# Kernel optimization log

Hardware: AMD Instinct MI355X
Metric: run time of the kernel (lower is better)

## Reference

```python
import jax, jax.numpy as jnp
import numpy as np

B, T, C, H = 2, 2048, 768, 12
HD = C // H  # head dim = 64
EPS = 1e-5


def layer_norm(x, g, b):
    mu = jnp.mean(x, axis=-1, keepdims=True)
    var = jnp.var(x, axis=-1, keepdims=True)
    return (x - mu) * jax.lax.rsqrt(var + EPS) * g + b


def setup_inputs() -> dict:
    key = jax.random.key(0)
    ks = jax.random.split(key, 5)
    s = 0.02
    return {
        "x": jax.random.normal(ks[0], (B, T, C), jnp.float32),
        "ln1_g": jnp.ones((C,), jnp.float32),
        "ln1_b": jnp.zeros((C,), jnp.float32),
        "W_qkv": jax.random.normal(ks[1], (C, 3 * C), jnp.float32) * s,
        "W_attn_proj": jax.random.normal(ks[2], (C, C), jnp.float32) * s,
        "ln2_g": jnp.ones((C,), jnp.float32),
        "ln2_b": jnp.zeros((C,), jnp.float32),
        "W_fc": jax.random.normal(ks[3], (C, 4 * C), jnp.float32) * s,
        "W_mlp_proj": jax.random.normal(ks[4], (4 * C, C), jnp.float32) * s,
    }


def attention(x, W_qkv, W_attn_proj):
    b, t, c = x.shape
    qkv = x @ W_qkv  # [B,T,3C]
    q, k, v = jnp.split(qkv, 3, axis=-1)
    # [B,H,T,HD]
    q = q.reshape(b, t, H, HD).transpose(0, 2, 1, 3)
    k = k.reshape(b, t, H, HD).transpose(0, 2, 1, 3)
    v = v.reshape(b, t, H, HD).transpose(0, 2, 1, 3)
    att = jnp.einsum("bhqd,bhkd->bhqk", q, k) * (1.0 / np.sqrt(HD).astype(np.float32))
    causal = jnp.tril(jnp.ones((t, t), jnp.bool_))
    att = jnp.where(causal, att, jnp.finfo(att.dtype).min)
    att = jax.nn.softmax(att, axis=-1)
    y = jnp.einsum("bhqk,bhkd->bhqd", att, v)
    y = y.transpose(0, 2, 1, 3).reshape(b, t, c)
    return y @ W_attn_proj


def mlp(x, W_fc, W_mlp_proj):
    h = jax.nn.gelu(x @ W_fc, approximate=False)
    return h @ W_mlp_proj


def reference(x, ln1_g, ln1_b, W_qkv, W_attn_proj, ln2_g, ln2_b, W_fc, W_mlp_proj):
    x = x + attention(layer_norm(x, ln1_g, ln1_b), W_qkv, W_attn_proj)
    x = x + mlp(layer_norm(x, ln2_g, ln2_b), W_fc, W_mlp_proj)
    return x
```

## Files before the change

kernel.cpp:

```cpp
#include <hip/hip_runtime.h>
#include <cstdint>
#include <cstddef>

typedef unsigned short u16;
typedef __attribute__((ext_vector_type(4))) float f32x4;
typedef __attribute__((ext_vector_type(8))) short bf16x8;

__device__ __forceinline__ u16 f2bf(float f) {
  unsigned int u = __builtin_bit_cast(unsigned int, f);
  u += 0x7fffu + ((u >> 16) & 1u);
  return (u16)(u >> 16);
}

__device__ __forceinline__ void gl_lds16(const u16* g, u16* lds_base) {
  __builtin_amdgcn_global_load_lds(
      (const __attribute__((address_space(1))) unsigned int*)g,
      (__attribute__((address_space(3))) unsigned int*)lds_base, 16, 0, 0);
}

__global__ __launch_bounds__(256) void transpose_all(const float* __restrict__ s0,
                                                     const float* __restrict__ s1,
                                                     const float* __restrict__ s2,
                                                     const float* __restrict__ s3,
                                                     u16* __restrict__ d0,
                                                     u16* __restrict__ d1,
                                                     u16* __restrict__ d2,
                                                     u16* __restrict__ d3) {
  __shared__ float tile[32][33];
  int idx = blockIdx.x;
  const float* src; u16* dst; int K, N, t;
  if (idx < 1728)      { src = s0; dst = d0; K = 768;  N = 2304; t = idx; }
  else if (idx < 2304) { src = s1; dst = d1; K = 768;  N = 768;  t = idx - 1728; }
  else if (idx < 4608) { src = s2; dst = d2; K = 768;  N = 3072; t = idx - 2304; }
  else                 { src = s3; dst = d3; K = 3072; N = 768;  t = idx - 4608; }
  int nt_n = N >> 5;
  int n0 = (t % nt_n) * 32, k0 = (t / nt_n) * 32;
  int tx = threadIdx.x & 31, ty = threadIdx.x >> 5;
#pragma unroll
  for (int i = 0; i < 4; ++i)
    tile[ty + i * 8][tx] = src[(size_t)(k0 + ty + i * 8) * N + n0 + tx];
  __syncthreads();
#pragma unroll
  for (int i = 0; i < 4; ++i)
    dst[(size_t)(n0 + ty + i * 8) * K + k0 + tx] = f2bf(tile[tx][ty + i * 8]);
}

__global__ __launch_bounds__(256) void transpose_v(const u16* __restrict__ qkvb,
                                                   u16* __restrict__ vt,
                                                   unsigned int* __restrict__ ctr) {
  __shared__ u16 tile[64 * 72];
  if (blockIdx.x == 0 && blockIdx.y == 0 && threadIdx.x == 0) *ctr = 0u;
  int t0 = blockIdx.x * 64;
  int bh = blockIdx.y;
  int b = bh / 12, h = bh % 12;
  int tid = threadIdx.x;
  int c8 = tid & 7, r = tid >> 3;
#pragma unroll
  for (int i = 0; i < 2; ++i) {
    int rr = r + i * 32;
    *(uint4*)&tile[rr * 72 + c8 * 8] =
        *(const uint4*)&qkvb[(size_t)(b * 2048 + t0 + rr) * 2304 + 1536 + h * 64 + c8 * 8];
  }
  __syncthreads();
#pragma unroll
  for (int i = 0; i < 2; ++i) {
    int dr = r + i * 32;
    u16 tmp[8];
#pragma unroll
    for (int j = 0; j < 8; ++j) tmp[j] = tile[(c8 * 8 + j) * 72 + dr];
    *(uint4*)&vt[((size_t)bh * 64 + dr) * 2048 + t0 + c8 * 8] = *(uint4*)tmp;
  }
}

__global__ __launch_bounds__(192) void ln_rows(const float* __restrict__ x,
                                               const float* __restrict__ g,
                                               const float* __restrict__ bb,
                                               u16* __restrict__ out) {
  int row = blockIdx.x;
  int t = threadIdx.x;
  float4 v = *(const float4*)(x + (size_t)row * 768 + t * 4);
  float s = v.x + v.y + v.z + v.w;
  float sq = v.x * v.x + v.y * v.y + v.z * v.z + v.w * v.w;
#pragma unroll
  for (int o = 32; o > 0; o >>= 1) {
    s += __shfl_down(s, o);
    sq += __shfl_down(sq, o);
  }
  __shared__ float ss[3], s2[3];
  int w = t >> 6;
  if ((t & 63) == 0) { ss[w] = s; s2[w] = sq; }
  __syncthreads();
  s = ss[0] + ss[1] + ss[2];
  sq = s2[0] + s2[1] + s2[2];
  float mu = s * (1.f / 768.f);
  float var = sq * (1.f / 768.f) - mu * mu;
  float rs = rsqrtf(var + 1e-5f);
  float4 gv = *(const float4*)(g + t * 4);
  float4 bv = *(const float4*)(bb + t * 4);
  u16 o4[4];
  o4[0] = f2bf((v.x - mu) * rs * gv.x + bv.x);
  o4[1] = f2bf((v.y - mu) * rs * gv.y + bv.y);
  o4[2] = f2bf((v.z - mu) * rs * gv.z + bv.z);
  o4[3] = f2bf((v.w - mu) * rs * gv.w + bv.w);
  *(uint2*)(out + (size_t)row * 768 + t * 4) = *(uint2*)o4;
}

template <int EPI, int TM>
__global__ __launch_bounds__(256, 3) void gemm_bt(const u16* __restrict__ A,
                                                  const u16* __restrict__ BT,
                                                  int M, int N, int K,
                                                  float* __restrict__ outF,
                                                  u16* __restrict__ outB,
                                                  const float* __restrict__ res) {
  constexpr int MT = TM / 64;
  __shared__ __align__(16) u16 Al[2][TM * 64];
  __shared__ __align__(16) u16 Bl[2][64 * 64];
  int tid = threadIdx.x;
  int lane = tid & 63, w = tid >> 6;
  int l16 = lane & 15, quad = lane >> 4;
  int swz = l16 & 7;

  int gx = gridDim.x;
  int nwg = gx * gridDim.y;
  int wg = blockIdx.y * gx + blockIdx.x;
  int chunk = nwg >> 3;
  int swg = (wg & 7) * chunk + (wg >> 3);
  int bx = swg % gx, by = swg / gx;

  size_t rowA0 = (size_t)by * TM;
  size_t rowB0 = (size_t)bx * 64;

  auto stage = [&](int buf, int k0) {
#pragma unroll
    for (int i = 0; i < TM / 32; ++i) {
      int cbase = (i * 4 + w) * 64;
      int chunk2 = cbase + lane;
      int r = chunk2 >> 3, c8 = (chunk2 & 7) ^ (r & 7);
      gl_lds16(&A[(rowA0 + r) * (size_t)K + k0 + c8 * 8], &Al[buf][cbase * 8]);
    }
#pragma unroll
    for (int i = 0; i < 2; ++i) {
      int cbase = (i * 4 + w) * 64;
      int chunk2 = cbase + lane;
      int r = chunk2 >> 3, c8 = (chunk2 & 7) ^ (r & 7);
      gl_lds16(&BT[(rowB0 + r) * (size_t)K + k0 + c8 * 8], &Bl[buf][cbase * 8]);
    }
  };

  f32x4 acc[MT][4] = {};
  stage(0, 0);
  int cur = 0;
  for (int k0 = 0; k0 < K; k0 += 64) {
    __syncthreads();
    if (k0 + 64 < K) stage(cur ^ 1, k0 + 64);
#pragma unroll
    for (int ks = 0; ks < 2; ++ks) {
      int c = ks * 4 + quad;
      bf16x8 af[MT], bf[4];
#pragma unroll
      for (int mt = 0; mt < MT; ++mt)
        af[mt] = *(const bf16x8*)&Al[cur][(w * (TM / 4) + mt * 16 + l16) * 64 + (c ^ swz) * 8];
#pragma unroll
      for (int nt = 0; nt < 4; ++nt)
        bf[nt] = *(const bf16x8*)&Bl[cur][(nt * 16 + l16) * 64 + (c ^ swz) * 8];
#pragma unroll
      for (int mt = 0; mt < MT; ++mt)
#pragma unroll
        for (int nt = 0; nt < 4; ++nt)
          acc[mt][nt] = __builtin_amdgcn_mfma_f32_16x16x32_bf16(af[mt], bf[nt], acc[mt][nt], 0, 0, 0);
    }
    cur ^= 1;
  }

#pragma unroll
  for (int mt = 0; mt < MT; ++mt) {
#pragma unroll
    for (int i = 0; i < 4; ++i) {
      size_t row = rowA0 + w * (TM / 4) + mt * 16 + quad * 4 + i;
#pragma unroll
      for (int nt = 0; nt < 4; ++nt) {
        size_t col = rowB0 + nt * 16 + l16;
        float v = acc[mt][nt][i];
        if (EPI == 0) {
          outB[row * N + col] = f2bf(v);
        } else if (EPI == 1) {
          outF[row * N + col] = res[row * N + col] + v;
        } else {
          float ge = 0.5f * v * (1.f + erff(v * 0.70710678118654752f));
          outB[row * N + col] = f2bf(ge);
        }
      }
    }
  }
}

__global__ __launch_bounds__(256, 3) void flash_attn(const u16* __restrict__ qkv,
                                                     const u16* __restrict__ vt,
                                                     u16* __restrict__ y,
                                                     float* __restrict__ OP,
                                                     float* __restrict__ LP,
                                                     unsigned int* __restrict__ ctr) {
  __shared__ __align__(16) u16 Kl[128 * 64];
  __shared__ __align__(16) u16 Vl[64 * 128];
  __shared__ __align__(16) u16 Pl[4][16 * 136];
  __shared__ unsigned int s_unit;

  int tid = threadIdx.x;
  int lane = tid & 63, w = tid >> 6;
  int l16 = lane & 15, quad = lane >> 4;
  int swz = l16 & 7;
  u16* Pw = &Pl[w][0];

  for (;;) {
    __syncthreads();
    if (tid == 0) s_unit = atomicAdd(ctr, 1u);
    __syncthreads();
    unsigned int u = s_unit;
    if (u >= 1152u) return;

    int qt, bh, kb0, kb1, part;
    bool heavy;
    if (u < 384u) {
      int t = (int)u;
      qt = 31 - t / 24; bh = t % 24;
      part = 0; kb0 = 0; kb1 = 8; heavy = true;
    } else if (u < 768u) {
      int t = (int)u - 384;
      qt = 31 - t / 24; bh = t % 24;
      part = 1; kb0 = 8; kb1 = qt / 2 + 1; heavy = true;
    } else {
      int t = (int)u - 768;
      qt = 15 - t / 24; bh = t % 24;
      part = 0; kb0 = 0; kb1 = qt / 2 + 1; heavy = false;
    }
    int b = bh / 12, h = bh % 12;
    int qw = qt * 64 + w * 16;
    int kdiag = qt / 2;

    const u16* base = qkv + (size_t)b * 2048 * 2304;
    const u16* vbase = vt + (size_t)bh * 64 * 2048;

    bf16x8 qf0, qf1;
    {
      const u16* qp = base + (size_t)(qw + l16) * 2304 + h * 64 + quad * 8;
      qf0 = *(const bf16x8*)qp;
      qf1 = *(const bf16x8*)(qp + 32);
    }

    f32x4 O[4] = {};
    float l_i[4] = {0.f, 0.f, 0.f, 0.f};

    const float sc = 0.125f * 1.44269504088896340736f;

    auto stageK = [&](int kt0) {
#pragma unroll
      for (int i = 0; i < 4; ++i) {
        int cbase = (i * 4 + w) * 64;
        int chunk = cbase + lane;
        int r = chunk >> 3, c8 = (chunk & 7) ^ (r & 7);
        gl_lds16(base + (size_t)(kt0 + r) * 2304 + 768 + h * 64 + c8 * 8, &Kl[cbase * 8]);
      }
    };
    auto stageV = [&](int kt0) {
#pragma unroll
      for (int i = 0; i < 4; ++i) {
        int cbase = (i * 4 + w) * 64;
        int chunk = cbase + lane;
        int r = chunk >> 4, c16 = (chunk & 15) ^ (r & 7);
        gl_lds16(vbase + (size_t)r * 2048 + kt0 + c16 * 8, &Vl[cbase * 8]);
      }
    };

    stageK(kb0 << 7);
    for (int kb = kb0; kb < kb1; ++kb) {
      int kt0 = kb << 7;
      __syncthreads();
      stageV(kt0);

      f32x4 S[8];
#pragma unroll
      for (int nt = 0; nt < 8; ++nt) {
        bf16x8 k0 = *(const bf16x8*)&Kl[(nt * 16 + l16) * 64 + (quad ^ swz) * 8];
        bf16x8 k1 = *(const bf16x8*)&Kl[(nt * 16 + l16) * 64 + ((4 + quad) ^ swz) * 8];
        f32x4 z = {};
        z = __builtin_amdgcn_mfma_f32_16x16x32_bf16(qf0, k0, z, 0, 0, 0);
        S[nt] = __builtin_amdgcn_mfma_f32_16x16x32_bf16(qf1, k1, z, 0, 0, 0);
      }

      bool diag = (kb == kdiag);
#pragma unroll
      for (int nt = 0; nt < 8; ++nt) {
        int tk = kt0 + nt * 16 + l16;
#pragma unroll
        for (int i = 0; i < 4; ++i) {
          float p = exp2f(S[nt][i] * sc);
          if (diag && tk > qw + quad * 4 + i) p = 0.f;
          l_i[i] += p;
          Pw[(quad * 4 + i) * 136 + nt * 16 + l16] =
              (u16)(__builtin_bit_cast(unsigned int, p) >> 16);
        }
      }

      __syncthreads();
      if (kb + 1 < kb1) stageK((kb + 1) << 7);

#pragma unroll
      for (int c = 0; c < 4; ++c) {
        bf16x8 pf = *(const bf16x8*)&Pw[l16 * 136 + c * 32 + quad * 8];
#pragma unroll
        for (int dt = 0; dt < 4; ++dt) {
          bf16x8 vf = *(const bf16x8*)&Vl[(dt * 16 + l16) * 128 + ((c * 4 + quad) ^ swz) * 8];
          O[dt] = __builtin_amdgcn_mfma_f32_16x16x32_bf16(pf, vf, O[dt], 0, 0, 0);
        }
      }
    }

#pragma unroll
    for (int i = 0; i < 4; ++i) {
#pragma unroll
      for (int o = 1; o < 16; o <<= 1) l_i[i] += __shfl_xor(l_i[i], o);
    }

    if (heavy) {
      size_t tno = (size_t)(bh * 16 + (qt - 16)) * 2 + part;
      float* op = OP + tno * 4096;
      float* lp = LP + tno * 64;
#pragma unroll
      for (int dt = 0; dt < 4; ++dt) {
#pragma unroll
        for (int i = 0; i < 4; ++i)
          op[(w * 16 + quad * 4 + i) * 64 + dt * 16 + l16] = O[dt][i];
      }
      if (l16 == 0) {
#pragma unroll
        for (int i = 0; i < 4; ++i) lp[w * 16 + quad * 4 + i] = l_i[i];
      }
    } else {
#pragma unroll
      for (int dt = 0; dt < 4; ++dt) {
#pragma unroll
        for (int i = 0; i < 4; ++i) {
          int tq = qw + quad * 4 + i;
          float ov = O[dt][i] / l_i[i];
          y[(size_t)(b * 2048 + tq) * 768 + h * 64 + dt * 16 + l16] = f2bf(ov);
        }
      }
    }
  }
}

__global__ __launch_bounds__(256) void attn_combine(const float* __restrict__ OP,
                                                    const float* __restrict__ LP,
                                                    u16* __restrict__ y) {
  int t = blockIdx.x;
  int bh = t >> 4, qth = t & 15;
  int b = bh / 12, h = bh % 12;
  int tid = threadIdx.x;
  int r = tid >> 2;
  int c0 = (tid & 3) << 4;
  const float* a = OP + (size_t)t * 2 * 4096 + r * 64 + c0;
  const float* bp = a + 4096;
  float inv = 1.f / (LP[(size_t)t * 128 + r] + LP[(size_t)t * 128 + 64 + r]);
  u16 ob[16];
#pragma unroll
  for (int j = 0; j < 16; ++j) ob[j] = f2bf((a[j] + bp[j]) * inv);
  size_t row = (size_t)b * 2048 + (size_t)(16 + qth) * 64 + r;
  u16* yp = y + row * 768 + h * 64 + c0;
  *(uint4*)yp = *(uint4*)&ob[0];
  *(uint4*)(yp + 8) = *(uint4*)&ob[8];
}

extern "C" void kernel_launch(void* const* d_in, const int* in_sizes, int n_in,
                              void* d_out, int out_size, void* d_ws, size_t ws_size,
                              hipStream_t stream) {
  const float* x      = (const float*)d_in[0];
  const float* ln1_g  = (const float*)d_in[1];
  const float* ln1_b  = (const float*)d_in[2];
  const float* W_qkv  = (const float*)d_in[3];
  const float* W_attn = (const float*)d_in[4];
  const float* ln2_g  = (const float*)d_in[5];
  const float* ln2_b  = (const float*)d_in[6];
  const float* W_fc   = (const float*)d_in[7];
  const float* W_mlp  = (const float*)d_in[8];
  float* out = (float*)d_out;

  const int M = 4096;
  char* p = (char*)d_ws;
  auto alloc = [&](size_t bytes) {
    char* r = p;
    p += (bytes + 255) & ~(size_t)255;
    return r;
  };
  u16* wt_qkv  = (u16*)alloc((size_t)2304 * 768 * 2);
  u16* wt_attn = (u16*)alloc((size_t)768 * 768 * 2);
  u16* wt_fc   = (u16*)alloc((size_t)3072 * 768 * 2);
  u16* wt_mlp  = (u16*)alloc((size_t)768 * 3072 * 2);
  u16* xn1     = (u16*)alloc((size_t)M * 768 * 2);
  u16* qkvb    = (u16*)alloc((size_t)M * 2304 * 2);
  u16* yb      = (u16*)alloc((size_t)M * 768 * 2);
  float* x1    = (float*)alloc((size_t)M * 768 * 4);
  u16* xn2     = (u16*)alloc((size_t)M * 768 * 2);
  u16* hb      = (u16*)alloc((size_t)M * 3072 * 2);
  u16* vt      = (u16*)alloc((size_t)24 * 64 * 2048 * 2);
  unsigned int* ctr = (unsigned int*)alloc(256);

  float* OPb = (float*)hb;
  float* LPb = OPb + (size_t)24 * 16 * 2 * 4096;

  transpose_all<<<6912, 256, 0, stream>>>(W_qkv, W_attn, W_fc, W_mlp,
                                          wt_qkv, wt_attn, wt_fc, wt_mlp);

  ln_rows<<<M, 192, 0, stream>>>(x, ln1_g, ln1_b, xn1);
  gemm_bt<0, 128><<<dim3(2304 / 64, M / 128), 256, 0, stream>>>(xn1, wt_qkv, M, 2304, 768,
                                                                nullptr, qkvb, nullptr);
  transpose_v<<<dim3(32, 24), 256, 0, stream>>>(qkvb, vt, ctr);
  flash_attn<<<768, 256, 0, stream>>>(qkvb, vt, yb, OPb, LPb, ctr);
  attn_combine<<<384, 256, 0, stream>>>(OPb, LPb, yb);
  gemm_bt<1, 64><<<dim3(768 / 64, M / 64), 256, 0, stream>>>(yb, wt_attn, M, 768, 768,
                                                             x1, nullptr, x);
  ln_rows<<<M, 192, 0, stream>>>(x1, ln2_g, ln2_b, xn2);
  gemm_bt<2, 128><<<dim3(3072 / 64, M / 128), 256, 0, stream>>>(xn2, wt_fc, M, 3072, 768,
                                                                nullptr, hb, nullptr);
  gemm_bt<1, 64><<<dim3(768 / 64, M / 64), 256, 0, stream>>>(hb, wt_mlp, M, 768, 3072,
                                                             out, nullptr, x1);
}
```

Baseline: 267.6 us.

## Use 128-row query tiles with 8-wave blocks in flash attention

The flash attention kernel moves from 4-wave blocks on 64-row query tiles to 8-wave blocks on 128-row query tiles. Each staged 128-key K/V tile is now reused by twice as many query rows, which halves global-to-LDS staging traffic per query. The work-unit queue is rebuilt to interleave split second halves of heavy tiles with light single-pass tiles, and the combine kernel is resized to match. Risks are coarser load balance with fewer, larger units, more wasted masked work on the diagonal block, and lower occupancy per CU.

```diff
diff --git a/kernel.cpp b/kernel.cpp
--- a/kernel.cpp
+++ b/kernel.cpp
@@ -194,7 +194,7 @@
   }
 }
 
-__global__ __launch_bounds__(256, 3) void flash_attn(const u16* __restrict__ qkv,
+__global__ __launch_bounds__(512, 2) void flash_attn(const u16* __restrict__ qkv,
                                                      const u16* __restrict__ vt,
                                                      u16* __restrict__ y,
                                                      float* __restrict__ OP,
@@ -202,7 +202,7 @@
                                                      unsigned int* __restrict__ ctr) {
   __shared__ __align__(16) u16 Kl[128 * 64];
   __shared__ __align__(16) u16 Vl[64 * 128];
-  __shared__ __align__(16) u16 Pl[4][16 * 136];
+  __shared__ __align__(16) u16 Pl[8][16 * 136];
   __shared__ unsigned int s_unit;
 
   int tid = threadIdx.x;
@@ -216,26 +216,29 @@
     if (tid == 0) s_unit = atomicAdd(ctr, 1u);
     __syncthreads();
     unsigned int u = s_unit;
-    if (u >= 1152u) return;
-
-    int qt, bh, kb0, kb1, part;
-    bool heavy;
-    if (u < 384u) {
+    if (u >= 576u) return;
+
+    int qb, bh, kb0, kb1, part;
+    bool multi;
+    if (u < 192u) {
       int t = (int)u;
-      qt = 31 - t / 24; bh = t % 24;
-      part = 0; kb0 = 0; kb1 = 8; heavy = true;
-    } else if (u < 768u) {
-      int t = (int)u - 384;
-      qt = 31 - t / 24; bh = t % 24;
-      part = 1; kb0 = 8; kb1 = qt / 2 + 1; heavy = true;
+      qb = 15 - t / 24; bh = t % 24;
+      part = 0; kb0 = 0; kb1 = 8; multi = true;
     } else {
-      int t = (int)u - 768;
-      qt = 15 - t / 24; bh = t % 24;
-      part = 0; kb0 = 0; kb1 = qt / 2 + 1; heavy = false;
+      int t = (int)u - 192;
+      int s = 8 - t / 48;
+      int r2 = t % 48;
+      if (r2 < 24) {
+        qb = s + 7; bh = r2;
+        part = 1; kb0 = 8; kb1 = qb + 1; multi = true;
+      } else {
+        qb = s - 1; bh = r2 - 24;
+        part = 0; kb0 = 0; kb1 = qb + 1; multi = false;
+      }
     }
     int b = bh / 12, h = bh % 12;
-    int qw = qt * 64 + w * 16;
-    int kdiag = qt / 2;
+    int qw = qb * 128 + w * 16;
+    int kdiag = qb;
 
     const u16* base = qkv + (size_t)b * 2048 * 2304;
     const u16* vbase = vt + (size_t)bh * 64 * 2048;
@@ -254,8 +257,8 @@
 
     auto stageK = [&](int kt0) {
 #pragma unroll
-      for (int i = 0; i < 4; ++i) {
-        int cbase = (i * 4 + w) * 64;
+      for (int i = 0; i < 2; ++i) {
+        int cbase = (i * 8 + w) * 64;
         int chunk = cbase + lane;
         int r = chunk >> 3, c8 = (chunk & 7) ^ (r & 7);
         gl_lds16(base + (size_t)(kt0 + r) * 2304 + 768 + h * 64 + c8 * 8, &Kl[cbase * 8]);
@@ -263,8 +266,8 @@
     };
     auto stageV = [&](int kt0) {
 #pragma unroll
-      for (int i = 0; i < 4; ++i) {
-        int cbase = (i * 4 + w) * 64;
+      for (int i = 0; i < 2; ++i) {
+        int cbase = (i * 8 + w) * 64;
         int chunk = cbase + lane;
         int r = chunk >> 4, c16 = (chunk & 15) ^ (r & 7);
         gl_lds16(vbase + (size_t)r * 2048 + kt0 + c16 * 8, &Vl[cbase * 8]);
@@ -321,10 +324,10 @@
       for (int o = 1; o < 16; o <<= 1) l_i[i] += __shfl_xor(l_i[i], o);
     }
 
-    if (heavy) {
-      size_t tno = (size_t)(bh * 16 + (qt - 16)) * 2 + part;
-      float* op = OP + tno * 4096;
-      float* lp = LP + tno * 64;
+    if (multi) {
+      size_t tno = (size_t)(bh * 8 + (qb - 8)) * 2 + part;
+      float* op = OP + tno * 8192;
+      float* lp = LP + tno * 128;
 #pragma unroll
       for (int dt = 0; dt < 4; ++dt) {
 #pragma unroll
@@ -353,21 +356,23 @@
                                                     const float* __restrict__ LP,
                                                     u16* __restrict__ y) {
   int t = blockIdx.x;
-  int bh = t >> 4, qth = t & 15;
+  int bh = t >> 3, qbh = t & 7;
   int b = bh / 12, h = bh % 12;
   int tid = threadIdx.x;
-  int r = tid >> 2;
-  int c0 = (tid & 3) << 4;
-  const float* a = OP + (size_t)t * 2 * 4096 + r * 64 + c0;
-  const float* bp = a + 4096;
-  float inv = 1.f / (LP[(size_t)t * 128 + r] + LP[(size_t)t * 128 + 64 + r]);
-  u16 ob[16];
-#pragma unroll
-  for (int j = 0; j < 16; ++j) ob[j] = f2bf((a[j] + bp[j]) * inv);
-  size_t row = (size_t)b * 2048 + (size_t)(16 + qth) * 64 + r;
+  int r = tid >> 1;
+  int c0 = (tid & 1) << 5;
+  const float* a = OP + (size_t)t * 2 * 8192 + r * 64 + c0;
+  const float* bp = a + 8192;
+  float inv = 1.f / (LP[(size_t)t * 256 + r] + LP[(size_t)t * 256 + 128 + r]);
+  u16 ob[32];
+#pragma unroll
+  for (int j = 0; j < 32; ++j) ob[j] = f2bf((a[j] + bp[j]) * inv);
+  size_t row = (size_t)b * 2048 + (size_t)(8 + qbh) * 128 + r;
   u16* yp = y + row * 768 + h * 64 + c0;
   *(uint4*)yp = *(uint4*)&ob[0];
   *(uint4*)(yp + 8) = *(uint4*)&ob[8];
+  *(uint4*)(yp + 16) = *(uint4*)&ob[16];
+  *(uint4*)(yp + 24) = *(uint4*)&ob[24];
 }
 
 extern "C" void kernel_launch(void* const* d_in, const int* in_sizes, int n_in,
@@ -405,7 +410,7 @@
   unsigned int* ctr = (unsigned int*)alloc(256);
 
   float* OPb = (float*)hb;
-  float* LPb = OPb + (size_t)24 * 16 * 2 * 4096;
+  float* LPb = OPb + (size_t)384 * 8192;
 
   transpose_all<<<6912, 256, 0, stream>>>(W_qkv, W_attn, W_fc, W_mlp,
                                           wt_qkv, wt_attn, wt_fc, wt_mlp);
@@ -414,8 +419,8 @@
   gemm_bt<0, 128><<<dim3(2304 / 64, M / 128), 256, 0, stream>>>(xn1, wt_qkv, M, 2304, 768,
                                                                 nullptr, qkvb, nullptr);
   transpose_v<<<dim3(32, 24), 256, 0, stream>>>(qkvb, vt, ctr);
-  flash_attn<<<768, 256, 0, stream>>>(qkvb, vt, yb, OPb, LPb, ctr);
-  attn_combine<<<384, 256, 0, stream>>>(OPb, LPb, yb);
+  flash_attn<<<512, 512, 0, stream>>>(qkvb, vt, yb, OPb, LPb, ctr);
+  attn_combine<<<192, 256, 0, stream>>>(OPb, LPb, yb);
   gemm_bt<1, 64><<<dim3(768 / 64, M / 64), 256, 0, stream>>>(yb, wt_attn, M, 768, 768,
                                                              x1, nullptr, x);
   ln_rows<<<M, 192, 0, stream>>>(x1, ln2_g, ln2_b, xn2);
```

New measurement: 264.5 us. Within noise of the previous version (-1.2%).
